# Performance work log

Measured on AMD Instinct MI355X. Metric: run time of the kernel, lower is better.

Reference implementation:

```python
import jax, jax.numpy as jnp
import numpy as np

BATCH, SEQ, D_IN, D_HID, D_OUT = 256, 512, 128, 128, 128


def setup_inputs() -> dict:
    key = jax.random.key(0)
    ks = jax.random.split(key, 10)
    def xavier(k, shape):
        std = (2.0 / (shape[0] + shape[1])) ** 0.5
        return jax.random.normal(k, shape, dtype=jnp.float32) * std
    return {
        "x": jax.random.normal(ks[0], (BATCH, SEQ, D_IN), dtype=jnp.float32),
        "x2i": xavier(ks[1], (D_IN, D_HID)),
        "x2f": xavier(ks[2], (D_IN, D_HID)),
        "x2g": xavier(ks[3], (D_IN, D_HID)),
        "x2o": xavier(ks[4], (D_IN, D_HID)),
        "h2i": xavier(ks[5], (D_HID, D_HID)),
        "h2f": xavier(ks[6], (D_HID, D_HID)),
        "h2g": xavier(ks[7], (D_HID, D_HID)),
        "h2o": xavier(ks[8], (D_HID, D_HID)),
        "w_out": xavier(ks[9], (D_HID, D_OUT)),
    }


def reference(x, x2i, x2f, x2g, x2o, h2i, h2f, h2g, h2o, w_out):
    batch = x.shape[0]
    hid = h2i.shape[0]
    # Precompute input projections for all timesteps (same math, hoisted out
    # of the recurrence): [B, S, 4H] -> time-major [S, B, 4H]
    wx = jnp.concatenate([x2i, x2f, x2g, x2o], axis=1)       # [D_IN, 4H]
    wh = jnp.concatenate([h2i, h2f, h2g, h2o], axis=1)       # [H, 4H]
    xg = jnp.einsum("bsi,ik->sbk", x, wx)                    # [S, B, 4H]

    def step(carry, xg_t):
        c, h = carry
        gates = xg_t + h @ wh                                # [B, 4H]
        i = jax.nn.sigmoid(gates[:, 0 * hid:1 * hid])
        f = jax.nn.sigmoid(gates[:, 1 * hid:2 * hid])
        g = jnp.tanh(gates[:, 2 * hid:3 * hid])
        o = jax.nn.sigmoid(gates[:, 3 * hid:4 * hid])
        c = f * c + i * g
        h = o * jnp.tanh(c)
        return (c, h), None

    c0 = jnp.zeros((batch, hid), dtype=x.dtype)
    h0 = jnp.zeros((batch, hid), dtype=x.dtype)
    (c_T, h_T), _ = jax.lax.scan(step, (c0, h0), xg)
    return h_T @ w_out
```

## Files before the change

### kernel.cpp

```cpp
#include <hip/hip_runtime.h>

typedef unsigned int u32;
typedef __fp16 half2_t __attribute__((ext_vector_type(2)));
typedef __fp16 half8_t __attribute__((ext_vector_type(8)));
typedef float  f32x4   __attribute__((ext_vector_type(4)));
typedef int    i32x4   __attribute__((ext_vector_type(4)));

#define DIN 128
#define DH  128
#define SEQL 512
#define NBATCH 256
#define NC  512
#define TC  64
#define NCHUNK (SEQL/TC)

#define HOFF 131072
#define HF2  (131072 + 256)
#define LDS_TOTAL (131072 + 256 + 256)

__device__ __forceinline__ u32 pk2(float a, float b) {
  half2_t h = __builtin_amdgcn_cvt_pkrtz(a, b);
  return __builtin_bit_cast(u32, h);
}

__device__ __forceinline__ float fexp2(float x) {
#if defined(__has_builtin) && __has_builtin(__builtin_amdgcn_exp2f)
  return __builtin_amdgcn_exp2f(x);
#else
  return __builtin_exp2f(x);
#endif
}

__device__ __forceinline__ void step_barrier() {
  asm volatile("s_waitcnt lgkmcnt(0)" ::: "memory");
  __builtin_amdgcn_s_barrier();
  asm volatile("" ::: "memory");
}

#define MF(A, B, C) __builtin_amdgcn_mfma_f32_16x16x32_f16( \
    __builtin_bit_cast(half8_t, A), __builtin_bit_cast(half8_t, B), C, 0, 0, 0)
#define MFI8(A, B, C) __builtin_amdgcn_mfma_i32_16x16x64_i8( \
    __builtin_bit_cast(i32x4, A), __builtin_bit_cast(i32x4, B), C, 0, 0, 0)

__global__ void pack_w(const float* __restrict__ x2i, const float* __restrict__ x2f,
                       const float* __restrict__ x2g, const float* __restrict__ x2o,
                       u32* __restrict__ wxT) {
  int idx = blockIdx.x * blockDim.x + threadIdx.x;
  if (idx >= NC * 64) return;
  int j = idx >> 6, kk = idx & 63;
  int g = j >> 7, jjj = j & 127;
  const float* wx = (g == 0) ? x2i : (g == 1) ? x2f : (g == 2) ? x2g : x2o;
  float s = (g == 2) ? -2.885390082f : -1.442695041f;
  wxT[idx] = pk2(s * wx[(2*kk)*DH + jjj], s * wx[(2*kk+1)*DH + jjj]);
}

__global__ void pack_whi8(const float* __restrict__ h2i, const float* __restrict__ h2f,
                          const float* __restrict__ h2g, const float* __restrict__ h2o,
                          u32* __restrict__ whI, float* __restrict__ dqs) {
  int j = blockIdx.x * blockDim.x + threadIdx.x;
  if (j >= NC) return;
  int g = j >> 7, jj = j & 127;
  const float* wh = (g == 0) ? h2i : (g == 1) ? h2f : (g == 2) ? h2g : h2o;
  float amax = 1e-20f;
  for (int k = 0; k < DH; ++k) amax = fmaxf(amax, fabsf(wh[k*DH + jj]));
  float s = 127.f / amax;
  for (int kk = 0; kk < 32; ++kk) {
    u32 wword = 0;
#pragma unroll
    for (int t = 0; t < 4; ++t) {
      int q = (int)__builtin_rintf(wh[(4*kk + t)*DH + jj] * s);
      wword |= ((u32)(q & 0xFF)) << (8 * t);
    }
    whI[j*32 + kk] = wword;
  }
  dqs[j] = (amax / 16129.f) * ((g == 2) ? -2.885390082f : -1.442695041f);
}

__global__ __launch_bounds__(512, 2)
void lstm_fused(
    const float* __restrict__ x, const u32* __restrict__ wxT,
    const u32* __restrict__ whI, const float* __restrict__ dqs,
    const float* __restrict__ w_out, float* __restrict__ out) {
  extern __shared__ char lds[];

  const int tid = threadIdx.x;
  const int b   = blockIdx.x;
  const int l   = tid & 63, wv = tid >> 6;
  const int kg  = l >> 4, r15 = l & 15;
  const int j   = wv * 16 + r15;

  uint4 bi8[4][2];
#pragma unroll
  for (int g = 0; g < 4; ++g) {
    const uint4* wp = (const uint4*)(whI + (g * DH + j) * 32);
    bi8[g][0] = wp[kg];
    bi8[g][1] = wp[4 + kg];
  }
  const float dqo = dqs[kg * DH + j];
  const float cA = (kg == 2) ? 2.f : 1.f;
  const float cB = (kg == 2) ? -1.f : 0.f;
  uint4 bfA[4][4];
#pragma unroll
  for (int nt = 0; nt < 4; ++nt) {
    int n = wv * 64 + nt * 16 + r15;
#pragma unroll
    for (int ko = 0; ko < 4; ++ko)
      bfA[nt][ko] = *(const uint4*)(wxT + n*64 + ko*16 + kg*4);
  }

  if (tid < 64) ((u32*)(lds + HOFF))[tid] = 0u;
  float c = 0.f, lasth = 0.f;
  u32 rdh = HOFF;
  u32 wrh = HOFF + 128;
  const float* xb = x + (size_t)b * SEQL * DIN;
  const f32x4 Z  = {0.f, 0.f, 0.f, 0.f};
  const i32x4 ZI = {0, 0, 0, 0};
  __syncthreads();

#pragma unroll 1
  for (int tt = 0; tt < 4; ++tt) {
    uint4 afr0[4];
#pragma unroll
    for (int ko = 0; ko < 4; ++ko) {
      const float4* xp = (const float4*)(xb + (size_t)(tt*16 + r15)*DIN + ko*32 + kg*8);
      float4 v0 = xp[0], v1 = xp[1];
      afr0[ko].x = pk2(v0.x, v0.y); afr0[ko].y = pk2(v0.z, v0.w);
      afr0[ko].z = pk2(v1.x, v1.y); afr0[ko].w = pk2(v1.z, v1.w);
    }
#pragma unroll
    for (int nt = 0; nt < 4; ++nt) {
      int n = wv * 64 + nt * 16 + r15;
      f32x4 acc = MF(afr0[0], bfA[nt][0], Z);
      acc = MF(afr0[1], bfA[nt][1], acc);
      acc = MF(afr0[2], bfA[nt][2], acc);
      acc = MF(afr0[3], bfA[nt][3], acc);
      int t0 = tt*16 + kg*4;
      u32 off = (u32)(n*128 + ((t0*2) ^ ((n & 7) << 4)));
      uint2 pw; pw.x = pk2(acc[0], acc[1]); pw.y = pk2(acc[2], acc[3]);
      *(uint2*)(lds + off) = pw;
    }
  }
  __syncthreads();

  int cur = 0;
#pragma unroll 1
  for (int ch = 0; ch < NCHUNK; ++ch) {
    char* xgC = lds + cur * 65536;
    char* xgN = lds + (cur ^ 1) * 65536;
    const bool doA = (ch + 1 < NCHUNK);
    float4 lv[8];
    uint4  afr[4];
    f32x4  aacc;

#pragma unroll 1
    for (int m = 0; m < 8; ++m) {
      const int tt = m >> 1;
      const int cg = kg * DH + j;
      half8_t xh = __builtin_bit_cast(half8_t,
          *(const uint4*)(xgC + cg*128 + ((m*16) ^ ((cg & 7) << 4))));
#pragma unroll
      for (int s8 = 0; s8 < 8; ++s8) {
        if (doA) {
          if ((m & 1) == 0) {
            if (s8 == 0) {
              const float* xr = xb + (size_t)((ch+1)*TC + tt*16 + r15)*DIN + kg*8;
#pragma unroll
              for (int ko = 0; ko < 4; ++ko) {
                const float4* xp = (const float4*)(xr + ko*32);
                lv[2*ko]   = xp[0];
                lv[2*ko+1] = xp[1];
              }
            }
            if (s8 == 2) {
#pragma unroll
              for (int ko = 0; ko < 2; ++ko) {
                float4 v0 = lv[2*ko], v1 = lv[2*ko+1];
                afr[ko].x = pk2(v0.x, v0.y); afr[ko].y = pk2(v0.z, v0.w);
                afr[ko].z = pk2(v1.x, v1.y); afr[ko].w = pk2(v1.z, v1.w);
              }
            }
            if (s8 == 3) {
#pragma unroll
              for (int ko = 2; ko < 4; ++ko) {
                float4 v0 = lv[2*ko], v1 = lv[2*ko+1];
                afr[ko].x = pk2(v0.x, v0.y); afr[ko].y = pk2(v0.z, v0.w);
                afr[ko].z = pk2(v1.x, v1.y); afr[ko].w = pk2(v1.z, v1.w);
              }
            }
          } else {
            const int nt = s8 >> 1;
            if ((s8 & 1) == 0) {
              aacc = MF(afr[1], bfA[nt][1], MF(afr[0], bfA[nt][0], Z));
            } else {
              aacc = MF(afr[3], bfA[nt][3], MF(afr[2], bfA[nt][2], aacc));
              int n = wv * 64 + nt * 16 + r15;
              int t0 = tt*16 + kg*4;
              u32 off = (u32)(n*128 + ((t0*2) ^ ((n & 7) << 4)));
              uint2 pw; pw.x = pk2(aacc[0], aacc[1]); pw.y = pk2(aacc[2], aacc[3]);
              *(uint2*)(xgN + off) = pw;
            }
          }
        }

        uint4 a0 = *(const uint4*)(lds + rdh + kg*16);
        uint4 a1 = *(const uint4*)(lds + rdh + 64 + kg*16);
        i32x4 aci = MFI8(a0, bi8[0][0], ZI);
        i32x4 acf = MFI8(a0, bi8[1][0], ZI);
        i32x4 acg = MFI8(a0, bi8[2][0], ZI);
        i32x4 aco = MFI8(a0, bi8[3][0], ZI);
        aci = MFI8(a1, bi8[0][1], aci);
        acf = MFI8(a1, bi8[1][1], acf);
        acg = MFI8(a1, bi8[2][1], acg);
        aco = MFI8(a1, bi8[3][1], aco);
        int aown = (kg == 0) ? aci[0] : (kg == 1) ? acf[0]
                 : (kg == 2) ? acg[0] : aco[0];
        float g0 = __builtin_fmaf((float)aown, dqo, (float)xh[s8]);
        float y  = __builtin_amdgcn_rcpf(1.f + fexp2(g0));
        float s  = __builtin_fmaf(cA, y, cB);
        float sf_ = __shfl_xor(s, 16, 64);
        float sg_ = __shfl_xor(s, 32, 64);
        float so_ = __shfl_xor(s, 48, 64);
        c = __builtin_fmaf(sf_, c, s * sg_);
        float th = __builtin_fmaf(2.f,
                     __builtin_amdgcn_rcpf(1.f + fexp2(c * -2.885390082f)), -1.f);
        float hval = so_ * th;
        lasth = hval;
        int q = (int)__builtin_rintf(hval * 127.f);
        if (l < 16) *(char*)(lds + wrh + j) = (char)q;
        u32 tswap = rdh; rdh = wrh; wrh = tswap;
        step_barrier();
      }
    }
    cur ^= 1;
  }

  if (l < 16) *(__fp16*)(lds + HF2 + j * 2) = (__fp16)lasth;
  __syncthreads();
  if (tid < DH) {
    int n = tid;
    const u32* hf = (const u32*)(lds + HF2);
    float acc = 0.f;
#pragma unroll 8
    for (int kk = 0; kk < 64; ++kk) {
      half2_t h2v = __builtin_bit_cast(half2_t, hf[kk]);
      acc = __builtin_fmaf((float)h2v[0], w_out[(2*kk)*DH + n],
            __builtin_fmaf((float)h2v[1], w_out[(2*kk+1)*DH + n], acc));
    }
    out[b * DH + n] = acc;
  }
}

extern "C" void kernel_launch(void* const* d_in, const int* in_sizes, int n_in,
                              void* d_out, int out_size, void* d_ws, size_t ws_size,
                              hipStream_t stream) {
  const float* x    = (const float*)d_in[0];
  const float* x2i  = (const float*)d_in[1];
  const float* x2f  = (const float*)d_in[2];
  const float* x2g  = (const float*)d_in[3];
  const float* x2o  = (const float*)d_in[4];
  const float* h2i  = (const float*)d_in[5];
  const float* h2f  = (const float*)d_in[6];
  const float* h2g  = (const float*)d_in[7];
  const float* h2o  = (const float*)d_in[8];
  const float* wout = (const float*)d_in[9];

  u32*   wxT = (u32*)d_ws;
  u32*   whI = wxT + NC * 64;
  float* dqs = (float*)(whI + NC * 32);

  (void)hipFuncSetAttribute((const void*)lstm_fused,
                            hipFuncAttributeMaxDynamicSharedMemorySize, LDS_TOTAL);

  pack_w<<<64, 512, 0, stream>>>(x2i, x2f, x2g, x2o, wxT);
  pack_whi8<<<1, 512, 0, stream>>>(h2i, h2f, h2g, h2o, whI, dqs);
  lstm_fused<<<NBATCH, 512, LDS_TOTAL, stream>>>(x, wxT, whI, dqs, wout, (float*)d_out);
}
```

Before: 258.9 us.

## Process two batch sequences per workgroup to interleave independent recurrences

```diff
diff --git a/kernel.cpp b/kernel.cpp
--- a/kernel.cpp
+++ b/kernel.cpp
@@ -11,12 +11,12 @@
 #define SEQL 512
 #define NBATCH 256
 #define NC  512
-#define TC  64
+#define TC  32
 #define NCHUNK (SEQL/TC)
 
 #define HOFF 131072
-#define HF2  (131072 + 256)
-#define LDS_TOTAL (131072 + 256 + 256)
+#define HF2  (131072 + 512)
+#define LDS_TOTAL (131072 + 1024)
 
 __device__ __forceinline__ u32 pk2(float a, float b) {
   half2_t h = __builtin_amdgcn_cvt_pkrtz(a, b);
@@ -29,6 +29,10 @@
 #else
   return __builtin_exp2f(x);
 #endif
+}
+
+__device__ __forceinline__ u32 swz(int col) {
+  return ((u32)((col ^ (col >> 2)) & 3)) << 4;
 }
 
 __device__ __forceinline__ void step_barrier() {
@@ -84,7 +88,7 @@
   extern __shared__ char lds[];
 
   const int tid = threadIdx.x;
-  const int b   = blockIdx.x;
+  const int b0  = blockIdx.x * 2, b1 = b0 + 1;
   const int l   = tid & 63, wv = tid >> 6;
   const int kg  = l >> 4, r15 = l & 15;
   const int j   = wv * 16 + r15;
@@ -108,36 +112,42 @@
       bfA[nt][ko] = *(const uint4*)(wxT + n*64 + ko*16 + kg*4);
   }
 
-  if (tid < 64) ((u32*)(lds + HOFF))[tid] = 0u;
-  float c = 0.f, lasth = 0.f;
-  u32 rdh = HOFF;
-  u32 wrh = HOFF + 128;
-  const float* xb = x + (size_t)b * SEQL * DIN;
+  if (tid < 128) ((u32*)(lds + HOFF))[tid] = 0u;
+  float c0 = 0.f, c1 = 0.f, lasth0 = 0.f, lasth1 = 0.f;
+  u32 rdh0 = HOFF,       wrh0 = HOFF + 128;
+  u32 rdh1 = HOFF + 256, wrh1 = HOFF + 384;
+  const float* xb0 = x + (size_t)b0 * SEQL * DIN;
+  const float* xb1 = x + (size_t)b1 * SEQL * DIN;
   const f32x4 Z  = {0.f, 0.f, 0.f, 0.f};
   const i32x4 ZI = {0, 0, 0, 0};
   __syncthreads();
 
 #pragma unroll 1
-  for (int tt = 0; tt < 4; ++tt) {
-    uint4 afr0[4];
-#pragma unroll
-    for (int ko = 0; ko < 4; ++ko) {
-      const float4* xp = (const float4*)(xb + (size_t)(tt*16 + r15)*DIN + ko*32 + kg*8);
-      float4 v0 = xp[0], v1 = xp[1];
-      afr0[ko].x = pk2(v0.x, v0.y); afr0[ko].y = pk2(v0.z, v0.w);
-      afr0[ko].z = pk2(v1.x, v1.y); afr0[ko].w = pk2(v1.z, v1.w);
-    }
-#pragma unroll
-    for (int nt = 0; nt < 4; ++nt) {
-      int n = wv * 64 + nt * 16 + r15;
-      f32x4 acc = MF(afr0[0], bfA[nt][0], Z);
-      acc = MF(afr0[1], bfA[nt][1], acc);
-      acc = MF(afr0[2], bfA[nt][2], acc);
-      acc = MF(afr0[3], bfA[nt][3], acc);
-      int t0 = tt*16 + kg*4;
-      u32 off = (u32)(n*128 + ((t0*2) ^ ((n & 7) << 4)));
-      uint2 pw; pw.x = pk2(acc[0], acc[1]); pw.y = pk2(acc[2], acc[3]);
-      *(uint2*)(lds + off) = pw;
+  for (int e = 0; e < 2; ++e) {
+    const float* xbe = e ? xb1 : xb0;
+    char* dst = lds + e * 65536;
+#pragma unroll 1
+    for (int tt = 0; tt < 2; ++tt) {
+      uint4 afr0[4];
+#pragma unroll
+      for (int ko = 0; ko < 4; ++ko) {
+        const float4* xp = (const float4*)(xbe + (size_t)(tt*16 + r15)*DIN + ko*32 + kg*8);
+        float4 v0 = xp[0], v1 = xp[1];
+        afr0[ko].x = pk2(v0.x, v0.y); afr0[ko].y = pk2(v0.z, v0.w);
+        afr0[ko].z = pk2(v1.x, v1.y); afr0[ko].w = pk2(v1.z, v1.w);
+      }
+#pragma unroll
+      for (int nt = 0; nt < 4; ++nt) {
+        int n = wv * 64 + nt * 16 + r15;
+        f32x4 acc = MF(afr0[0], bfA[nt][0], Z);
+        acc = MF(afr0[1], bfA[nt][1], acc);
+        acc = MF(afr0[2], bfA[nt][2], acc);
+        acc = MF(afr0[3], bfA[nt][3], acc);
+        int t0 = tt*16 + kg*4;
+        u32 off = (u32)(n*64 + ((t0*2) ^ swz(n)));
+        uint2 pw; pw.x = pk2(acc[0], acc[1]); pw.y = pk2(acc[2], acc[3]);
+        *(uint2*)(dst + off) = pw;
+      }
     }
   }
   __syncthreads();
@@ -145,25 +155,29 @@
   int cur = 0;
 #pragma unroll 1
   for (int ch = 0; ch < NCHUNK; ++ch) {
-    char* xgC = lds + cur * 65536;
-    char* xgN = lds + (cur ^ 1) * 65536;
+    char* xgC0 = lds + cur * 32768;
+    char* xgC1 = lds + 65536 + cur * 32768;
+    char* xgN0 = lds + (cur ^ 1) * 32768;
+    char* xgN1 = lds + 65536 + (cur ^ 1) * 32768;
     const bool doA = (ch + 1 < NCHUNK);
     float4 lv[8];
-    uint4  afr[4];
-    f32x4  aacc;
+    uint4  afrA[4], afrB[4];
+    f32x4  aaccA, aaccB;
 
 #pragma unroll 1
-    for (int m = 0; m < 8; ++m) {
+    for (int m = 0; m < 4; ++m) {
       const int tt = m >> 1;
       const int cg = kg * DH + j;
-      half8_t xh = __builtin_bit_cast(half8_t,
-          *(const uint4*)(xgC + cg*128 + ((m*16) ^ ((cg & 7) << 4))));
+      half8_t xh0 = __builtin_bit_cast(half8_t,
+          *(const uint4*)(xgC0 + cg*64 + ((m*16) ^ swz(cg))));
+      half8_t xh1 = __builtin_bit_cast(half8_t,
+          *(const uint4*)(xgC1 + cg*64 + ((m*16) ^ swz(cg))));
 #pragma unroll
       for (int s8 = 0; s8 < 8; ++s8) {
         if (doA) {
           if ((m & 1) == 0) {
             if (s8 == 0) {
-              const float* xr = xb + (size_t)((ch+1)*TC + tt*16 + r15)*DIN + kg*8;
+              const float* xr = xb0 + (size_t)((ch+1)*TC + tt*16 + r15)*DIN + kg*8;
 #pragma unroll
               for (int ko = 0; ko < 4; ++ko) {
                 const float4* xp = (const float4*)(xr + ko*32);
@@ -175,70 +189,128 @@
 #pragma unroll
               for (int ko = 0; ko < 2; ++ko) {
                 float4 v0 = lv[2*ko], v1 = lv[2*ko+1];
-                afr[ko].x = pk2(v0.x, v0.y); afr[ko].y = pk2(v0.z, v0.w);
-                afr[ko].z = pk2(v1.x, v1.y); afr[ko].w = pk2(v1.z, v1.w);
+                afrA[ko].x = pk2(v0.x, v0.y); afrA[ko].y = pk2(v0.z, v0.w);
+                afrA[ko].z = pk2(v1.x, v1.y); afrA[ko].w = pk2(v1.z, v1.w);
               }
             }
             if (s8 == 3) {
 #pragma unroll
               for (int ko = 2; ko < 4; ++ko) {
                 float4 v0 = lv[2*ko], v1 = lv[2*ko+1];
-                afr[ko].x = pk2(v0.x, v0.y); afr[ko].y = pk2(v0.z, v0.w);
-                afr[ko].z = pk2(v1.x, v1.y); afr[ko].w = pk2(v1.z, v1.w);
+                afrA[ko].x = pk2(v0.x, v0.y); afrA[ko].y = pk2(v0.z, v0.w);
+                afrA[ko].z = pk2(v1.x, v1.y); afrA[ko].w = pk2(v1.z, v1.w);
+              }
+            }
+            if (s8 == 4) {
+              const float* xr = xb1 + (size_t)((ch+1)*TC + tt*16 + r15)*DIN + kg*8;
+#pragma unroll
+              for (int ko = 0; ko < 4; ++ko) {
+                const float4* xp = (const float4*)(xr + ko*32);
+                lv[2*ko]   = xp[0];
+                lv[2*ko+1] = xp[1];
+              }
+            }
+            if (s8 == 6) {
+#pragma unroll
+              for (int ko = 0; ko < 2; ++ko) {
+                float4 v0 = lv[2*ko], v1 = lv[2*ko+1];
+                afrB[ko].x = pk2(v0.x, v0.y); afrB[ko].y = pk2(v0.z, v0.w);
+                afrB[ko].z = pk2(v1.x, v1.y); afrB[ko].w = pk2(v1.z, v1.w);
+              }
+            }
+            if (s8 == 7) {
+#pragma unroll
+              for (int ko = 2; ko < 4; ++ko) {
+                float4 v0 = lv[2*ko], v1 = lv[2*ko+1];
+                afrB[ko].x = pk2(v0.x, v0.y); afrB[ko].y = pk2(v0.z, v0.w);
+                afrB[ko].z = pk2(v1.x, v1.y); afrB[ko].w = pk2(v1.z, v1.w);
               }
             }
           } else {
             const int nt = s8 >> 1;
             if ((s8 & 1) == 0) {
-              aacc = MF(afr[1], bfA[nt][1], MF(afr[0], bfA[nt][0], Z));
+              aaccA = MF(afrA[1], bfA[nt][1], MF(afrA[0], bfA[nt][0], Z));
+              aaccB = MF(afrB[1], bfA[nt][1], MF(afrB[0], bfA[nt][0], Z));
             } else {
-              aacc = MF(afr[3], bfA[nt][3], MF(afr[2], bfA[nt][2], aacc));
+              aaccA = MF(afrA[3], bfA[nt][3], MF(afrA[2], bfA[nt][2], aaccA));
+              aaccB = MF(afrB[3], bfA[nt][3], MF(afrB[2], bfA[nt][2], aaccB));
               int n = wv * 64 + nt * 16 + r15;
               int t0 = tt*16 + kg*4;
-              u32 off = (u32)(n*128 + ((t0*2) ^ ((n & 7) << 4)));
-              uint2 pw; pw.x = pk2(aacc[0], aacc[1]); pw.y = pk2(aacc[2], aacc[3]);
-              *(uint2*)(xgN + off) = pw;
+              u32 off = (u32)(n*64 + ((t0*2) ^ swz(n)));
+              uint2 pwA; pwA.x = pk2(aaccA[0], aaccA[1]); pwA.y = pk2(aaccA[2], aaccA[3]);
+              uint2 pwB; pwB.x = pk2(aaccB[0], aaccB[1]); pwB.y = pk2(aaccB[2], aaccB[3]);
+              *(uint2*)(xgN0 + off) = pwA;
+              *(uint2*)(xgN1 + off) = pwB;
             }
           }
         }
 
-        uint4 a0 = *(const uint4*)(lds + rdh + kg*16);
-        uint4 a1 = *(const uint4*)(lds + rdh + 64 + kg*16);
-        i32x4 aci = MFI8(a0, bi8[0][0], ZI);
-        i32x4 acf = MFI8(a0, bi8[1][0], ZI);
-        i32x4 acg = MFI8(a0, bi8[2][0], ZI);
-        i32x4 aco = MFI8(a0, bi8[3][0], ZI);
-        aci = MFI8(a1, bi8[0][1], aci);
-        acf = MFI8(a1, bi8[1][1], acf);
-        acg = MFI8(a1, bi8[2][1], acg);
-        aco = MFI8(a1, bi8[3][1], aco);
-        int aown = (kg == 0) ? aci[0] : (kg == 1) ? acf[0]
-                 : (kg == 2) ? acg[0] : aco[0];
-        float g0 = __builtin_fmaf((float)aown, dqo, (float)xh[s8]);
-        float y  = __builtin_amdgcn_rcpf(1.f + fexp2(g0));
-        float s  = __builtin_fmaf(cA, y, cB);
-        float sf_ = __shfl_xor(s, 16, 64);
-        float sg_ = __shfl_xor(s, 32, 64);
-        float so_ = __shfl_xor(s, 48, 64);
-        c = __builtin_fmaf(sf_, c, s * sg_);
-        float th = __builtin_fmaf(2.f,
-                     __builtin_amdgcn_rcpf(1.f + fexp2(c * -2.885390082f)), -1.f);
-        float hval = so_ * th;
-        lasth = hval;
-        int q = (int)__builtin_rintf(hval * 127.f);
-        if (l < 16) *(char*)(lds + wrh + j) = (char)q;
-        u32 tswap = rdh; rdh = wrh; wrh = tswap;
+        uint4 p0 = *(const uint4*)(lds + rdh0 + kg*16);
+        uint4 p1 = *(const uint4*)(lds + rdh0 + 64 + kg*16);
+        uint4 q0 = *(const uint4*)(lds + rdh1 + kg*16);
+        uint4 q1 = *(const uint4*)(lds + rdh1 + 64 + kg*16);
+        i32x4 ai0 = MFI8(p0, bi8[0][0], ZI);
+        i32x4 af0 = MFI8(p0, bi8[1][0], ZI);
+        i32x4 ag0 = MFI8(p0, bi8[2][0], ZI);
+        i32x4 ao0 = MFI8(p0, bi8[3][0], ZI);
+        i32x4 ai1 = MFI8(q0, bi8[0][0], ZI);
+        i32x4 af1 = MFI8(q0, bi8[1][0], ZI);
+        i32x4 ag1 = MFI8(q0, bi8[2][0], ZI);
+        i32x4 ao1 = MFI8(q0, bi8[3][0], ZI);
+        ai0 = MFI8(p1, bi8[0][1], ai0);
+        af0 = MFI8(p1, bi8[1][1], af0);
+        ag0 = MFI8(p1, bi8[2][1], ag0);
+        ao0 = MFI8(p1, bi8[3][1], ao0);
+        ai1 = MFI8(q1, bi8[0][1], ai1);
+        af1 = MFI8(q1, bi8[1][1], af1);
+        ag1 = MFI8(q1, bi8[2][1], ag1);
+        ao1 = MFI8(q1, bi8[3][1], ao1);
+        int aw0 = (kg == 0) ? ai0[0] : (kg == 1) ? af0[0]
+                : (kg == 2) ? ag0[0] : ao0[0];
+        float g0 = __builtin_fmaf((float)aw0, dqo, (float)xh0[s8]);
+        float y0 = __builtin_amdgcn_rcpf(1.f + fexp2(g0));
+        float s0 = __builtin_fmaf(cA, y0, cB);
+        float sf0 = __shfl_xor(s0, 16, 64);
+        float sg0 = __shfl_xor(s0, 32, 64);
+        float so0 = __shfl_xor(s0, 48, 64);
+        c0 = __builtin_fmaf(sf0, c0, s0 * sg0);
+        float th0 = __builtin_fmaf(2.f,
+                      __builtin_amdgcn_rcpf(1.f + fexp2(c0 * -2.885390082f)), -1.f);
+        float hv0 = so0 * th0;
+        lasth0 = hv0;
+        int qz0 = (int)__builtin_rintf(hv0 * 127.f);
+        if (l < 16) *(char*)(lds + wrh0 + j) = (char)qz0;
+        int aw1 = (kg == 0) ? ai1[0] : (kg == 1) ? af1[0]
+                : (kg == 2) ? ag1[0] : ao1[0];
+        float g1 = __builtin_fmaf((float)aw1, dqo, (float)xh1[s8]);
+        float y1 = __builtin_amdgcn_rcpf(1.f + fexp2(g1));
+        float s1 = __builtin_fmaf(cA, y1, cB);
+        float sf1 = __shfl_xor(s1, 16, 64);
+        float sg1 = __shfl_xor(s1, 32, 64);
+        float so1 = __shfl_xor(s1, 48, 64);
+        c1 = __builtin_fmaf(sf1, c1, s1 * sg1);
+        float th1 = __builtin_fmaf(2.f,
+                      __builtin_amdgcn_rcpf(1.f + fexp2(c1 * -2.885390082f)), -1.f);
+        float hv1 = so1 * th1;
+        lasth1 = hv1;
+        int qz1 = (int)__builtin_rintf(hv1 * 127.f);
+        if (l < 16) *(char*)(lds + wrh1 + j) = (char)qz1;
+        u32 t0s = rdh0; rdh0 = wrh0; wrh0 = t0s;
+        u32 t1s = rdh1; rdh1 = wrh1; wrh1 = t1s;
         step_barrier();
       }
     }
     cur ^= 1;
   }
 
-  if (l < 16) *(__fp16*)(lds + HF2 + j * 2) = (__fp16)lasth;
+  if (l < 16) {
+    *(__fp16*)(lds + HF2 + j * 2)       = (__fp16)lasth0;
+    *(__fp16*)(lds + HF2 + 256 + j * 2) = (__fp16)lasth1;
+  }
   __syncthreads();
-  if (tid < DH) {
-    int n = tid;
-    const u32* hf = (const u32*)(lds + HF2);
+  if (tid < 2 * DH) {
+    int e = tid >> 7, n = tid & 127;
+    const u32* hf = (const u32*)(lds + HF2 + e * 256);
     float acc = 0.f;
 #pragma unroll 8
     for (int kk = 0; kk < 64; ++kk) {
@@ -246,7 +318,7 @@
       acc = __builtin_fmaf((float)h2v[0], w_out[(2*kk)*DH + n],
             __builtin_fmaf((float)h2v[1], w_out[(2*kk+1)*DH + n], acc));
     }
-    out[b * DH + n] = acc;
+    out[(e ? b1 : b0) * DH + n] = acc;
   }
 }
 
@@ -273,5 +345,5 @@
 
   pack_w<<<64, 512, 0, stream>>>(x2i, x2f, x2g, x2o, wxT);
   pack_whi8<<<1, 512, 0, stream>>>(h2i, h2f, h2g, h2o, whI, dqs);
-  lstm_fused<<<NBATCH, 512, LDS_TOTAL, stream>>>(x, wxT, whI, dqs, wout, (float*)d_out);
-}
+  lstm_fused<<<NBATCH/2, 512, LDS_TOTAL, stream>>>(x, wxT, whI, dqs, wout, (float*)d_out);
+}
```

New measurement: 425.6 us. 64.4% more time.

## Halve LSTM block to four waves, each computing two hidden-column groups

Applied to the files above, without the earlier changes.

```diff
diff --git a/kernel.cpp b/kernel.cpp
--- a/kernel.cpp
+++ b/kernel.cpp
@@ -76,7 +76,8 @@
   dqs[j] = (amax / 16129.f) * ((g == 2) ? -2.885390082f : -1.442695041f);
 }
 
-__global__ __launch_bounds__(512, 2)
+__global__ __launch_bounds__(256)
+__attribute__((amdgpu_waves_per_eu(1, 1)))
 void lstm_fused(
     const float* __restrict__ x, const u32* __restrict__ wxT,
     const u32* __restrict__ whI, const float* __restrict__ dqs,
@@ -87,29 +88,32 @@
   const int b   = blockIdx.x;
   const int l   = tid & 63, wv = tid >> 6;
   const int kg  = l >> 4, r15 = l & 15;
-  const int j   = wv * 16 + r15;
-
-  uint4 bi8[4][2];
+  const int jA  = wv * 32 + r15;
+  const int jB  = jA + 16;
+
+  uint4 bi8[4][2][2];
 #pragma unroll
   for (int g = 0; g < 4; ++g) {
-    const uint4* wp = (const uint4*)(whI + (g * DH + j) * 32);
-    bi8[g][0] = wp[kg];
-    bi8[g][1] = wp[4 + kg];
-  }
-  const float dqo = dqs[kg * DH + j];
+    const uint4* wpA = (const uint4*)(whI + (g * DH + jA) * 32);
+    const uint4* wpB = (const uint4*)(whI + (g * DH + jB) * 32);
+    bi8[g][0][0] = wpA[kg];  bi8[g][0][1] = wpA[4 + kg];
+    bi8[g][1][0] = wpB[kg];  bi8[g][1][1] = wpB[4 + kg];
+  }
+  const float dqoA = dqs[kg * DH + jA];
+  const float dqoB = dqs[kg * DH + jB];
   const float cA = (kg == 2) ? 2.f : 1.f;
   const float cB = (kg == 2) ? -1.f : 0.f;
-  uint4 bfA[4][4];
-#pragma unroll
-  for (int nt = 0; nt < 4; ++nt) {
-    int n = wv * 64 + nt * 16 + r15;
+  uint4 bfA[8][4];
+#pragma unroll
+  for (int nt = 0; nt < 8; ++nt) {
+    int n = wv * 128 + nt * 16 + r15;
 #pragma unroll
     for (int ko = 0; ko < 4; ++ko)
       bfA[nt][ko] = *(const uint4*)(wxT + n*64 + ko*16 + kg*4);
   }
 
   if (tid < 64) ((u32*)(lds + HOFF))[tid] = 0u;
-  float c = 0.f, lasth = 0.f;
+  float c0 = 0.f, c1 = 0.f, lasthA = 0.f, lasthB = 0.f;
   u32 rdh = HOFF;
   u32 wrh = HOFF + 128;
   const float* xb = x + (size_t)b * SEQL * DIN;
@@ -128,8 +132,8 @@
       afr0[ko].z = pk2(v1.x, v1.y); afr0[ko].w = pk2(v1.z, v1.w);
     }
 #pragma unroll
-    for (int nt = 0; nt < 4; ++nt) {
-      int n = wv * 64 + nt * 16 + r15;
+    for (int nt = 0; nt < 8; ++nt) {
+      int n = wv * 128 + nt * 16 + r15;
       f32x4 acc = MF(afr0[0], bfA[nt][0], Z);
       acc = MF(afr0[1], bfA[nt][1], acc);
       acc = MF(afr0[2], bfA[nt][2], acc);
@@ -150,14 +154,15 @@
     const bool doA = (ch + 1 < NCHUNK);
     float4 lv[8];
     uint4  afr[4];
-    f32x4  aacc;
 
 #pragma unroll 1
     for (int m = 0; m < 8; ++m) {
       const int tt = m >> 1;
-      const int cg = kg * DH + j;
-      half8_t xh = __builtin_bit_cast(half8_t,
-          *(const uint4*)(xgC + cg*128 + ((m*16) ^ ((cg & 7) << 4))));
+      const int cgA = kg * DH + jA, cgB = kg * DH + jB;
+      half8_t xhA = __builtin_bit_cast(half8_t,
+          *(const uint4*)(xgC + cgA*128 + ((m*16) ^ ((cgA & 7) << 4))));
+      half8_t xhB = __builtin_bit_cast(half8_t,
+          *(const uint4*)(xgC + cgB*128 + ((m*16) ^ ((cgB & 7) << 4))));
 #pragma unroll
       for (int s8 = 0; s8 < 8; ++s8) {
         if (doA) {
@@ -188,45 +193,68 @@
               }
             }
           } else {
-            const int nt = s8 >> 1;
-            if ((s8 & 1) == 0) {
-              aacc = MF(afr[1], bfA[nt][1], MF(afr[0], bfA[nt][0], Z));
-            } else {
-              aacc = MF(afr[3], bfA[nt][3], MF(afr[2], bfA[nt][2], aacc));
-              int n = wv * 64 + nt * 16 + r15;
-              int t0 = tt*16 + kg*4;
-              u32 off = (u32)(n*128 + ((t0*2) ^ ((n & 7) << 4)));
-              uint2 pw; pw.x = pk2(aacc[0], aacc[1]); pw.y = pk2(aacc[2], aacc[3]);
-              *(uint2*)(xgN + off) = pw;
-            }
+            const int nt = s8;
+            f32x4 aacc = MF(afr[0], bfA[nt][0], Z);
+            aacc = MF(afr[1], bfA[nt][1], aacc);
+            aacc = MF(afr[2], bfA[nt][2], aacc);
+            aacc = MF(afr[3], bfA[nt][3], aacc);
+            int n = wv * 128 + nt * 16 + r15;
+            int t0 = tt*16 + kg*4;
+            u32 off = (u32)(n*128 + ((t0*2) ^ ((n & 7) << 4)));
+            uint2 pw; pw.x = pk2(aacc[0], aacc[1]); pw.y = pk2(aacc[2], aacc[3]);
+            *(uint2*)(xgN + off) = pw;
           }
         }
 
         uint4 a0 = *(const uint4*)(lds + rdh + kg*16);
         uint4 a1 = *(const uint4*)(lds + rdh + 64 + kg*16);
-        i32x4 aci = MFI8(a0, bi8[0][0], ZI);
-        i32x4 acf = MFI8(a0, bi8[1][0], ZI);
-        i32x4 acg = MFI8(a0, bi8[2][0], ZI);
-        i32x4 aco = MFI8(a0, bi8[3][0], ZI);
-        aci = MFI8(a1, bi8[0][1], aci);
-        acf = MFI8(a1, bi8[1][1], acf);
-        acg = MFI8(a1, bi8[2][1], acg);
-        aco = MFI8(a1, bi8[3][1], aco);
-        int aown = (kg == 0) ? aci[0] : (kg == 1) ? acf[0]
-                 : (kg == 2) ? acg[0] : aco[0];
-        float g0 = __builtin_fmaf((float)aown, dqo, (float)xh[s8]);
-        float y  = __builtin_amdgcn_rcpf(1.f + fexp2(g0));
-        float s  = __builtin_fmaf(cA, y, cB);
-        float sf_ = __shfl_xor(s, 16, 64);
-        float sg_ = __shfl_xor(s, 32, 64);
-        float so_ = __shfl_xor(s, 48, 64);
-        c = __builtin_fmaf(sf_, c, s * sg_);
-        float th = __builtin_fmaf(2.f,
-                     __builtin_amdgcn_rcpf(1.f + fexp2(c * -2.885390082f)), -1.f);
-        float hval = so_ * th;
-        lasth = hval;
-        int q = (int)__builtin_rintf(hval * 127.f);
-        if (l < 16) *(char*)(lds + wrh + j) = (char)q;
+        i32x4 aiA = MFI8(a0, bi8[0][0][0], ZI);
+        i32x4 afA = MFI8(a0, bi8[1][0][0], ZI);
+        i32x4 agA = MFI8(a0, bi8[2][0][0], ZI);
+        i32x4 aoA = MFI8(a0, bi8[3][0][0], ZI);
+        i32x4 aiB = MFI8(a0, bi8[0][1][0], ZI);
+        i32x4 afB = MFI8(a0, bi8[1][1][0], ZI);
+        i32x4 agB = MFI8(a0, bi8[2][1][0], ZI);
+        i32x4 aoB = MFI8(a0, bi8[3][1][0], ZI);
+        aiA = MFI8(a1, bi8[0][0][1], aiA);
+        afA = MFI8(a1, bi8[1][0][1], afA);
+        agA = MFI8(a1, bi8[2][0][1], agA);
+        aoA = MFI8(a1, bi8[3][0][1], aoA);
+        aiB = MFI8(a1, bi8[0][1][1], aiB);
+        afB = MFI8(a1, bi8[1][1][1], afB);
+        agB = MFI8(a1, bi8[2][1][1], agB);
+        aoB = MFI8(a1, bi8[3][1][1], aoB);
+        int awA = (kg == 0) ? aiA[0] : (kg == 1) ? afA[0]
+                : (kg == 2) ? agA[0] : aoA[0];
+        int awB = (kg == 0) ? aiB[0] : (kg == 1) ? afB[0]
+                : (kg == 2) ? agB[0] : aoB[0];
+        float gA = __builtin_fmaf((float)awA, dqoA, (float)xhA[s8]);
+        float gB = __builtin_fmaf((float)awB, dqoB, (float)xhB[s8]);
+        float yA = __builtin_amdgcn_rcpf(1.f + fexp2(gA));
+        float yB = __builtin_amdgcn_rcpf(1.f + fexp2(gB));
+        float sA = __builtin_fmaf(cA, yA, cB);
+        float sB = __builtin_fmaf(cA, yB, cB);
+        float sfA = __shfl_xor(sA, 16, 64);
+        float sgA = __shfl_xor(sA, 32, 64);
+        float soA = __shfl_xor(sA, 48, 64);
+        float sfB = __shfl_xor(sB, 16, 64);
+        float sgB = __shfl_xor(sB, 32, 64);
+        float soB = __shfl_xor(sB, 48, 64);
+        c0 = __builtin_fmaf(sfA, c0, sA * sgA);
+        c1 = __builtin_fmaf(sfB, c1, sB * sgB);
+        float thA = __builtin_fmaf(2.f,
+                      __builtin_amdgcn_rcpf(1.f + fexp2(c0 * -2.885390082f)), -1.f);
+        float thB = __builtin_fmaf(2.f,
+                      __builtin_amdgcn_rcpf(1.f + fexp2(c1 * -2.885390082f)), -1.f);
+        float hvA = soA * thA;
+        float hvB = soB * thB;
+        lasthA = hvA; lasthB = hvB;
+        int qA = (int)__builtin_rintf(hvA * 127.f);
+        int qB = (int)__builtin_rintf(hvB * 127.f);
+        if (l < 16) {
+          *(char*)(lds + wrh + jA) = (char)qA;
+          *(char*)(lds + wrh + jB) = (char)qB;
+        }
         u32 tswap = rdh; rdh = wrh; wrh = tswap;
         step_barrier();
       }
@@ -234,7 +262,10 @@
     cur ^= 1;
   }
 
-  if (l < 16) *(__fp16*)(lds + HF2 + j * 2) = (__fp16)lasth;
+  if (l < 16) {
+    *(__fp16*)(lds + HF2 + jA * 2) = (__fp16)lasthA;
+    *(__fp16*)(lds + HF2 + jB * 2) = (__fp16)lasthB;
+  }
   __syncthreads();
   if (tid < DH) {
     int n = tid;
@@ -273,5 +304,5 @@
 
   pack_w<<<64, 512, 0, stream>>>(x2i, x2f, x2g, x2o, wxT);
   pack_whi8<<<1, 512, 0, stream>>>(h2i, h2f, h2g, h2o, whI, dqs);
-  lstm_fused<<<NBATCH, 512, LDS_TOTAL, stream>>>(x, wxT, whI, dqs, wout, (float*)d_out);
-}
+  lstm_fused<<<NBATCH, 256, LDS_TOTAL, stream>>>(x, wxT, whI, dqs, wout, (float*)d_out);
+}
```

Measured after the change: 329.0 us. 27.1% more time.
